# Kernel tuning notes

Hardware: AMD Instinct MI355X
Metric: run time of the kernel (lower is better)

Reference implementation:

```python
import jax, jax.numpy as jnp
import numpy as np

L = 2        # gnn_layers
D = 256      # hidden_dim
E = 1024     # emb_dim
NCLS = 7
NEG = 1e30


def lstm_cell(x, h, c, Wih, Whh, bih, bhh):
    # torch.nn.LSTMCell math; gate order i, f, g, o
    g = x @ Wih.T + bih + h @ Whh.T + bhh
    i, f, gg, o = jnp.split(g, 4, axis=-1)
    c2 = jax.nn.sigmoid(f) * c + jax.nn.sigmoid(i) * jnp.tanh(gg)
    return jax.nn.sigmoid(o) * jnp.tanh(c2), c2


def dag_layer(Hl, adj_f, W1, W2, Wr, Wc_ih, Wc_hh, bc_ih, bc_hh, Wp_ih, Wp_hh, bp_ih, bp_hh):
    # Hl: (B,N,D). Sequential DAG recurrence with dot-product attention over growing prefix.
    B, N, Dh = Hl.shape
    zeros = jnp.zeros((B, Dh), Hl.dtype)
    h0 = Hl[:, 0]
    C0, _ = lstm_cell(h0, zeros, zeros, Wc_ih, Wc_hh, bc_ih, bc_hh)
    P0, _ = lstm_cell(zeros, h0, h0, Wp_ih, Wp_hh, bp_ih, bp_hh)
    Ht0 = C0 + P0
    # carry pre-projected keys/values incrementally to avoid O(N^2 D^2) work
    K2 = jnp.zeros((B, N, Dh), Hl.dtype).at[:, 0].set(Ht0 @ W2.T)
    Vr = jnp.zeros((B, N, Dh), Hl.dtype).at[:, 0].set(Ht0 @ Wr.T)
    H1 = jnp.zeros((B, N, Dh), Hl.dtype).at[:, 0].set(Ht0)
    pos = jnp.arange(N)

    def step(carry, i):
        K2, Vr, H1 = carry
        Q = jax.lax.dynamic_index_in_dim(Hl, i, axis=1, keepdims=False)      # (B,D)
        adj_i = jax.lax.dynamic_index_in_dim(adj_f, i, axis=1, keepdims=False)  # (B,N)
        q = Q @ W1.T
        logits = jnp.einsum('bd,bnd->bn', q, K2) - (1.0 - adj_i) * NEG  # mask_logic
        logits = jnp.where(pos[None, :] < i, logits, -NEG)              # only prefix :i
        w = jax.nn.softmax(logits, axis=-1)
        M = jnp.einsum('bn,bnd->bd', w, Vr)
        C, _ = lstm_cell(Q, M, M, Wc_ih, Wc_hh, bc_ih, bc_hh)
        P, _ = lstm_cell(M, Q, Q, Wp_ih, Wp_hh, bp_ih, bp_hh)
        Ht = C + P
        K2 = K2.at[:, i].set(Ht @ W2.T)
        Vr = Vr.at[:, i].set(Ht @ Wr.T)
        H1 = H1.at[:, i].set(Ht)
        return (K2, Vr, H1), None

    (K2, Vr, H1), _ = jax.lax.scan(step, (K2, Vr, H1), jnp.arange(1, N))
    return H1


def setup_inputs() -> dict:
    key = jax.random.key(0)
    ks = iter(jax.random.split(key, 40))
    B, N = 16, 128
    s = lambda *sh: jax.random.normal(next(ks), sh, jnp.float32) * 0.02
    in_dim = D * (L + 1) + E
    return dict(
        features=jax.random.normal(next(ks), (B, N, E), jnp.float32),
        adj=jnp.ones((B, N, N), jnp.int32),
        s_mask=jnp.zeros((B, N, N), jnp.int32),
        s_mask_onehot=jnp.zeros((B, N, N, 2), jnp.int32),
        lengths=jnp.ones((B,), jnp.int32) * N,
        fc1_W=s(D, E), fc1_b=jnp.zeros((D,), jnp.float32),
        W1=s(L, D, D), W2=s(L, D, D), Wr=s(L, D, D),
        Wc_ih=s(L, 4 * D, D), Wc_hh=s(L, 4 * D, D),
        bc_ih=jnp.zeros((L, 4 * D), jnp.float32), bc_hh=jnp.zeros((L, 4 * D), jnp.float32),
        Wp_ih=s(L, 4 * D, D), Wp_hh=s(L, 4 * D, D),
        bp_ih=jnp.zeros((L, 4 * D), jnp.float32), bp_hh=jnp.zeros((L, 4 * D), jnp.float32),
        m0_W=s(D, in_dim), m0_b=jnp.zeros((D,), jnp.float32),
        m1_W=s(D, D), m1_b=jnp.zeros((D,), jnp.float32),
        m2_W=s(NCLS, D), m2_b=jnp.zeros((NCLS,), jnp.float32),
    )


def reference(features, adj, s_mask, s_mask_onehot, lengths,
              fc1_W, fc1_b, W1, W2, Wr,
              Wc_ih, Wc_hh, bc_ih, bc_hh,
              Wp_ih, Wp_hh, bp_ih, bp_hh,
              m0_W, m0_b, m1_W, m1_b, m2_W, m2_b):
    # s_mask / s_mask_onehot unused for attn_type='dotprod', no_rel_attn=True
    # lengths unused for nodal_att_type=None (attentive_node_features is identity)
    adj_f = adj.astype(features.dtype)
    H0 = jax.nn.relu(features @ fc1_W.T + fc1_b)
    Hs = [H0]
    for l in range(L):
        Hs.append(dag_layer(Hs[l], adj_f,
                            W1[l], W2[l], Wr[l],
                            Wc_ih[l], Wc_hh[l], bc_ih[l], bc_hh[l],
                            Wp_ih[l], Wp_hh[l], bp_ih[l], bp_hh[l]))
    Hcat = jnp.concatenate(Hs + [features], axis=2)  # (B,N,D*(L+1)+E)
    h = jax.nn.relu(Hcat @ m0_W.T + m0_b)
    h = jax.nn.relu(h @ m1_W.T + m1_b)  # mlp_layers-1 extra layer; dropout p=0 -> identity
    return h @ m2_W.T + m2_b            # (B,N,num_class)
```

## Files before the change

kernel.cpp:

```cpp
#include <hip/hip_runtime.h>
#include <hip/hip_fp16.h>
#include <math.h>

#define B_ 16
#define N_ 128
#define D_ 256
#define E_ 1024
#define GD4 1024
#define SENT 0xFFC0DEADu

typedef _Float16 h2 __attribute__((ext_vector_type(2)));

__device__ __forceinline__ float dot2w(unsigned w, h2 hv, float acc) {
#if __has_builtin(__builtin_amdgcn_fdot2)
  return __builtin_amdgcn_fdot2(__builtin_bit_cast(h2, w), hv, acc, false);
#else
  union { unsigned u; _Float16 e[2]; } c; c.u = w;
  return acc + (float)c.e[0]*(float)hv.x + (float)c.e[1]*(float)hv.y;
#endif
}
__device__ __forceinline__ float dot2h(h2 a, h2 b, float acc) {
#if __has_builtin(__builtin_amdgcn_fdot2)
  return __builtin_amdgcn_fdot2(a, b, acc, false);
#else
  return acc + (float)a.x*(float)b.x + (float)a.y*(float)b.y;
#endif
}

template<bool BIAS, bool RELU>
__global__ __launch_bounds__(256) void gemm_k(const float* __restrict__ X,
    const float* __restrict__ W, const float* __restrict__ bias,
    float* __restrict__ C, int M, int N, int K)
{
  __shared__ float Xs[32][68];
  __shared__ float Ws[32][68];
  const int tid = threadIdx.x;
  const int m0 = blockIdx.x * 64, n0 = blockIdx.y * 64;
  const int tm = tid >> 4, tn = tid & 15;
  float acc[4][4] = {};
  for (int k0 = 0; k0 < K; k0 += 32) {
    for (int e = tid; e < 2048; e += 256) {
      int mm = e >> 5, kk = e & 31;
      Xs[kk][mm] = X[(m0+mm)*K + k0+kk];
    }
    for (int e = tid; e < 2048; e += 256) {
      int nn = e >> 5, kk = e & 31;
      Ws[kk][nn] = (n0+nn < N) ? W[(n0+nn)*K + k0+kk] : 0.f;
    }
    __syncthreads();
    for (int kk = 0; kk < 32; kk++) {
      float4 a = *(const float4*)&Xs[kk][tm*4];
      float4 b = *(const float4*)&Ws[kk][tn*4];
      acc[0][0] += a.x*b.x; acc[0][1] += a.x*b.y; acc[0][2] += a.x*b.z; acc[0][3] += a.x*b.w;
      acc[1][0] += a.y*b.x; acc[1][1] += a.y*b.y; acc[1][2] += a.y*b.z; acc[1][3] += a.y*b.w;
      acc[2][0] += a.z*b.x; acc[2][1] += a.z*b.y; acc[2][2] += a.z*b.z; acc[2][3] += a.z*b.w;
      acc[3][0] += a.w*b.x; acc[3][1] += a.w*b.y; acc[3][2] += a.w*b.z; acc[3][3] += a.w*b.w;
    }
    __syncthreads();
  }
  for (int i2 = 0; i2 < 4; i2++) {
    int row = m0 + tm*4 + i2;
    for (int j2 = 0; j2 < 4; j2++) {
      int col = n0 + tn*4 + j2;
      if (col < N) {
        float v = acc[i2][j2];
        if (BIAS) v += bias[col];
        if (RELU) v = fmaxf(v, 0.f);
        C[row*N + col] = v;
      }
    }
  }
}

template<bool BIAS, bool RELU>
__global__ __launch_bounds__(256) void gemm16_k(const float* __restrict__ X,
    const float* __restrict__ W, const float* __restrict__ bias,
    float* __restrict__ C, int M, int N, int K)
{
  __shared__ h2 Xs2[16][68];
  __shared__ h2 Ws2[16][68];
  const int tid = threadIdx.x;
  const int m0 = blockIdx.x * 64, n0 = blockIdx.y * 64;
  const int tm = tid >> 4, tn = tid & 15;
  float acc[4][4] = {};
  for (int k0 = 0; k0 < K; k0 += 32) {
    for (int e = tid; e < 1024; e += 256) {
      int mm = e >> 4, p = e & 15;
      const float* xp = &X[(m0+mm)*K + k0 + 2*p];
      h2 t; t.x = (_Float16)xp[0]; t.y = (_Float16)xp[1];
      Xs2[p][mm] = t;
    }
    for (int e = tid; e < 1024; e += 256) {
      int nn = e >> 4, p = e & 15;
      const float* wp = &W[(n0+nn)*K + k0 + 2*p];
      h2 t; t.x = (_Float16)wp[0]; t.y = (_Float16)wp[1];
      Ws2[p][nn] = t;
    }
    __syncthreads();
    #pragma unroll 4
    for (int p = 0; p < 16; ++p) {
      h2 a[4], bb[4];
      *(float4*)a  = *(const float4*)&Xs2[p][tm*4];
      *(float4*)bb = *(const float4*)&Ws2[p][tn*4];
      #pragma unroll
      for (int i2 = 0; i2 < 4; i2++)
        #pragma unroll
        for (int j2 = 0; j2 < 4; j2++)
          acc[i2][j2] = dot2h(a[i2], bb[j2], acc[i2][j2]);
    }
    __syncthreads();
  }
  for (int i2 = 0; i2 < 4; i2++) {
    int row = m0 + tm*4 + i2;
    for (int j2 = 0; j2 < 4; j2++) {
      int col = n0 + tn*4 + j2;
      float v = acc[i2][j2];
      if (BIAS) v += bias[col];
      if (RELU) v = fmaxf(v, 0.f);
      C[row*N + col] = v;
    }
  }
}

__global__ __launch_bounds__(256) void prepamat_k(const float* __restrict__ W2,
    const float* __restrict__ W1, float* __restrict__ AM)
{
  __shared__ float Xs[32][68];
  __shared__ float Ws[32][68];
  const int tid = threadIdx.x;
  const int m0 = blockIdx.x * 64, n0 = blockIdx.y * 64;
  const float* X = W2 + blockIdx.z * 65536;
  const float* W = W1 + blockIdx.z * 65536;
  float* C = AM + blockIdx.z * 65536;
  const int tm = tid >> 4, tn = tid & 15;
  float acc[4][4] = {};
  for (int k0 = 0; k0 < 256; k0 += 32) {
    for (int e = tid; e < 2048; e += 256) {
      int kk = e >> 6, mm = e & 63;
      Xs[kk][mm] = X[(k0+kk)*256 + m0+mm];
    }
    for (int e = tid; e < 2048; e += 256) {
      int kk = e >> 6, nn = e & 63;
      Ws[kk][nn] = W[(k0+kk)*256 + n0+nn];
    }
    __syncthreads();
    for (int kk = 0; kk < 32; kk++) {
      float4 a = *(const float4*)&Xs[kk][tm*4];
      float4 b = *(const float4*)&Ws[kk][tn*4];
      acc[0][0] += a.x*b.x; acc[0][1] += a.x*b.y; acc[0][2] += a.x*b.z; acc[0][3] += a.x*b.w;
      acc[1][0] += a.y*b.x; acc[1][1] += a.y*b.y; acc[1][2] += a.y*b.z; acc[1][3] += a.y*b.w;
      acc[2][0] += a.z*b.x; acc[2][1] += a.z*b.y; acc[2][2] += a.z*b.z; acc[2][3] += a.z*b.w;
      acc[3][0] += a.w*b.x; acc[3][1] += a.w*b.y; acc[3][2] += a.w*b.z; acc[3][3] += a.w*b.w;
    }
    __syncthreads();
  }
  for (int i2 = 0; i2 < 4; i2++)
    for (int j2 = 0; j2 < 4; j2++)
      C[(m0 + tm*4 + i2)*256 + n0 + tn*4 + j2] = acc[i2][j2];
}

__global__ __launch_bounds__(256) void prepnn_k(const float* __restrict__ Wch,
    const float* __restrict__ Wpi, const float* __restrict__ Wr,
    float* __restrict__ OUT)
{
  __shared__ float Xs[32][68];
  __shared__ float Ws[32][68];
  const int tid = threadIdx.x;
  const int m0 = blockIdx.x * 64, n0 = blockIdx.y * 64;
  const int l = blockIdx.z;
  const float* X = (m0 < 1024) ? (Wch + l*262144 + m0*256)
                               : (Wpi + l*262144 + (m0-1024)*256);
  const float* W = Wr + l*65536;
  float* C = OUT + l*524288;
  const int tm = tid >> 4, tn = tid & 15;
  float acc[4][4] = {};
  for (int k0 = 0; k0 < 256; k0 += 32) {
    for (int e = tid; e < 2048; e += 256) {
      int mm = e >> 5, kk = e & 31;
      Xs[kk][mm] = X[mm*256 + k0+kk];
    }
    for (int e = tid; e < 2048; e += 256) {
      int kk = e >> 6, nn = e & 63;
      Ws[kk][nn] = W[(k0+kk)*256 + n0+nn];
    }
    __syncthreads();
    for (int kk = 0; kk < 32; kk++) {
      float4 a = *(const float4*)&Xs[kk][tm*4];
      float4 b = *(const float4*)&Ws[kk][tn*4];
      acc[0][0] += a.x*b.x; acc[0][1] += a.x*b.y; acc[0][2] += a.x*b.z; acc[0][3] += a.x*b.w;
      acc[1][0] += a.y*b.x; acc[1][1] += a.y*b.y; acc[1][2] += a.y*b.z; acc[1][3] += a.y*b.w;
      acc[2][0] += a.z*b.x; acc[2][1] += a.z*b.y; acc[2][2] += a.z*b.z; acc[2][3] += a.z*b.w;
      acc[3][0] += a.w*b.x; acc[3][1] += a.w*b.y; acc[3][2] += a.w*b.z; acc[3][3] += a.w*b.w;
    }
    __syncthreads();
  }
  for (int i2 = 0; i2 < 4; i2++)
    for (int j2 = 0; j2 < 4; j2++)
      C[(m0 + tm*4 + i2)*256 + n0 + tn*4 + j2] = acc[i2][j2];
}

__global__ void bias_sum_k(const float* __restrict__ bci, const float* __restrict__ bch,
                           const float* __restrict__ bpi, const float* __restrict__ bph,
                           float* __restrict__ bcC, float* __restrict__ bpC)
{
  int i = blockIdx.x*256 + threadIdx.x;
  if (i < 2048) { bcC[i] = bci[i] + bch[i]; bpC[i] = bpi[i] + bph[i]; }
}

__global__ void pack_k(const float* __restrict__ wchpi, const float* __restrict__ wr,
                       _Float16* __restrict__ out)
{
  int idx = blockIdx.x*256 + threadIdx.x;
  int l  = idx / 589824; int rem = idx % 589824;
  int sl = rem / 36864;  int rem2 = rem % 36864;
  int cq = rem2 / 1152;  int rem3 = rem2 % 1152;
  int r  = rem3 >> 3;    int e = rem3 & 7;
  int c  = cq*8 + e;
  int g  = r >> 4, dl = r & 15;
  int d  = sl*16 + dl;
  float v;
  if (g < 8) v = wchpi[l*524288 + (g*256 + d)*256 + c];
  else       v = wr[l*65536 + d*256 + c];
  out[idx] = (_Float16)v;
}

__global__ void fill_k(unsigned* __restrict__ a, unsigned* __restrict__ b)
{
  int i = blockIdx.x*256 + threadIdx.x;
  if (i < 524288) {
    __hip_atomic_store(a + i, SENT, __ATOMIC_RELAXED, __HIP_MEMORY_SCOPE_AGENT);
    __hip_atomic_store(b + i, SENT, __ATOMIC_RELAXED, __HIP_MEMORY_SCOPE_AGENT);
  }
}

__global__ __launch_bounds__(256) void prologue16_k(const float* __restrict__ X,
    const float* __restrict__ Wc, const float* __restrict__ Wp,
    const float* __restrict__ Am, const float* __restrict__ bcc,
    const float* __restrict__ bpc, float* __restrict__ GQC,
    float* __restrict__ GQP, float* __restrict__ VM)
{
  __shared__ h2 Xs2[16][68];
  __shared__ h2 Ws2[16][68];
  const int tid = threadIdx.x;
  const int m0 = blockIdx.x * 64;
  const int nt = blockIdx.y;
  const float* W; const float* bias; float* C; int n0; int NC;
  if (nt < 16)      { W = Wc; bias = bcc;     C = GQC; n0 = nt*64;      NC = 1024; }
  else if (nt < 32) { W = Wp; bias = bpc;     C = GQP; n0 = (nt-16)*64; NC = 1024; }
  else              { W = Am; bias = nullptr; C = VM;  n0 = (nt-32)*64; NC = 256;  }
  const int tm = tid >> 4, tn = tid & 15;
  float acc[4][4] = {};
  for (int k0 = 0; k0 < 256; k0 += 32) {
    for (int e = tid; e < 1024; e += 256) {
      int mm = e >> 4, p = e & 15;
      const float* xp = &X[(m0+mm)*256 + k0 + 2*p];
      h2 t; t.x = (_Float16)xp[0]; t.y = (_Float16)xp[1];
      Xs2[p][mm] = t;
    }
    for (int e = tid; e < 1024; e += 256) {
      int nn = e >> 4, p = e & 15;
      const float* wp = &W[(n0+nn)*256 + k0 + 2*p];
      h2 t; t.x = (_Float16)wp[0]; t.y = (_Float16)wp[1];
      Ws2[p][nn] = t;
    }
    __syncthreads();
    #pragma unroll 4
    for (int p = 0; p < 16; ++p) {
      h2 a[4], bb[4];
      *(float4*)a  = *(const float4*)&Xs2[p][tm*4];
      *(float4*)bb = *(const float4*)&Ws2[p][tn*4];
      #pragma unroll
      for (int i2 = 0; i2 < 4; i2++)
        #pragma unroll
        for (int j2 = 0; j2 < 4; j2++)
          acc[i2][j2] = dot2h(a[i2], bb[j2], acc[i2][j2]);
    }
    __syncthreads();
  }
  for (int i2 = 0; i2 < 4; i2++) {
    int row = m0 + tm*4 + i2;
    for (int j2 = 0; j2 < 4; j2++) {
      int col = n0 + tn*4 + j2;
      float v = acc[i2][j2];
      if (bias) v += bias[col];
      C[row*NC + col] = v;
    }
  }
}

__global__ __launch_bounds__(256) void m0fused16_k(const float* __restrict__ H0,
    const float* __restrict__ H1, const float* __restrict__ H2,
    const float* __restrict__ feat, const float* __restrict__ W,
    const float* __restrict__ bias, float* __restrict__ C)
{
  __shared__ h2 Xs2[16][68];
  __shared__ h2 Ws2[16][68];
  const int tid = threadIdx.x;
  const int m0 = blockIdx.x * 64, n0 = blockIdx.y * 64;
  const int tm = tid >> 4, tn = tid & 15;
  float acc[4][4] = {};
  for (int k0 = 0; k0 < 1792; k0 += 32) {
    for (int e = tid; e < 1024; e += 256) {
      int mm = e >> 4, p = e & 15;
      int k = k0 + 2*p, row = m0 + mm;
      float x0, x1;
      if (k < 768) {
        const float* src = (k < 256) ? H0 : ((k < 512) ? H1 : H2);
        x0 = src[row*256 + (k & 255)];
        x1 = src[row*256 + (k & 255) + 1];
      } else {
        x0 = feat[row*1024 + (k - 768)];
        x1 = feat[row*1024 + (k - 767)];
      }
      h2 t; t.x = (_Float16)x0; t.y = (_Float16)x1;
      Xs2[p][mm] = t;
    }
    for (int e = tid; e < 1024; e += 256) {
      int nn = e >> 4, p = e & 15;
      const float* wp = &W[(n0+nn)*1792 + k0 + 2*p];
      h2 t; t.x = (_Float16)wp[0]; t.y = (_Float16)wp[1];
      Ws2[p][nn] = t;
    }
    __syncthreads();
    #pragma unroll 4
    for (int p = 0; p < 16; ++p) {
      h2 a[4], bb[4];
      *(float4*)a  = *(const float4*)&Xs2[p][tm*4];
      *(float4*)bb = *(const float4*)&Ws2[p][tn*4];
      #pragma unroll
      for (int i2 = 0; i2 < 4; i2++)
        #pragma unroll
        for (int j2 = 0; j2 < 4; j2++)
          acc[i2][j2] = dot2h(a[i2], bb[j2], acc[i2][j2]);
    }
    __syncthreads();
  }
  for (int i2 = 0; i2 < 4; i2++) {
    int row = m0 + tm*4 + i2;
    for (int j2 = 0; j2 < 4; j2++) {
      int col = n0 + tn*4 + j2;
      C[row*256 + col] = fmaxf(acc[i2][j2] + bias[col], 0.f);
    }
  }
}

__device__ __forceinline__ float sigf(float x) { return 1.f / (1.f + __expf(-x)); }
__device__ __forceinline__ float tanhfast(float x) {
  float xc = fminf(fmaxf(x, -15.f), 15.f);
  float e = __expf(-2.f * xc);
  return (1.f - e) / (1.f + e);
}

__global__ __launch_bounds__(512, 2) void scan_k(
    const float* __restrict__ Hl,
    const float* __restrict__ Vm,
    const float* __restrict__ gqC,
    const float* __restrict__ gqP,
    const _Float16* __restrict__ WTp,
    const int*   __restrict__ adj,
    float* __restrict__ Hout)
{
  __shared__ uint4 wl4[4608];
  __shared__ float G[128*144];
  __shared__ __align__(16) _Float16 h2s[256];
  __shared__ float v_s[256];
  __shared__ __align__(16) _Float16 v2s[256];
  __shared__ float psum[128];
  __shared__ float aw[128];
  __shared__ int   adj_s[2][128];
  __shared__ float gqc_l[2][64], gqp_l[2][64];
  __shared__ float ql[2][16];
  __shared__ float Gg[144];
  __shared__ float red[2];
  __shared__ float sinv;

  const int tid = threadIdx.x;
  const int b   = blockIdx.x >> 4;
  const int sl  = blockIdx.x & 15;

  { const uint4* src = (const uint4*)WTp + (size_t)sl*4608;
    for (int e = tid; e < 4608; e += 512) wl4[e] = src[e]; }

  const int rr_ = tid >> 2;
  const int rj  = tid & 3;

#define PREF(ip_, bf_) do {                                                    \
    int ip = (ip_); int bf = (bf_);                                            \
    for (int u = tid - 288; u < 528; u += 224) {                               \
      if (u < 256) { float v = Vm[(b*N_ + ip)*D_ + u]; v_s[u] = v;             \
                     v2s[u] = (_Float16)v; }                                   \
      else if (u < 384) adj_s[bf][u-256] = adj[(b*N_ + ip)*N_ + (u-256)];      \
      else if (u < 448) gqc_l[bf][u-384] = gqC[(b*N_+ip)*GD4 + ((u-384)>>4)*D_ + sl*16 + ((u-384)&15)]; \
      else if (u < 512) gqp_l[bf][u-448] = gqP[(b*N_+ip)*GD4 + ((u-448)>>4)*D_ + sl*16 + ((u-448)&15)]; \
      else ql[bf][u-512] = Hl[(b*N_+ip)*D_ + sl*16 + (u-512)];                 \
    }                                                                          \
  } while (0)

  if (tid >= 288) PREF(0, 0);
  __syncthreads();

  for (int i = 0; i < N_; ++i) {
    const int cur = i & 1;
    if (i > 0) {
      if (rr_ + 1 < i) {
        const float4* hp = (const float4*)(Hout + ((size_t)(b*N_ + rr_))*D_) + rj;
        const float4* vv = (const float4*)v_s + rj;
        float4 areg[16];
        #pragma unroll
        for (int c4 = 0; c4 < 16; ++c4) areg[c4] = hp[c4*4];
        float acc = 0.f;
        #pragma unroll
        for (int c4 = 0; c4 < 16; ++c4) {
          float4 a = areg[c4], w = vv[c4*4];
          acc += a.x*w.x + a.y*w.y + a.z*w.z + a.w*w.w;
        }
        acc += __shfl_xor(acc, 1, 64);
        acc += __shfl_xor(acc, 2, 64);
        if (rj == 0) psum[rr_] = acc;
      }
      if (tid >= 448) {
        const unsigned* wp = (const unsigned*)Hout
                           + ((size_t)(b*N_ + (i-1)))*D_ + ((tid-448)&15)*16 + 15;
        while (__hip_atomic_load(wp, __ATOMIC_RELAXED, __HIP_MEMORY_SCOPE_AGENT) == SENT)
          __builtin_amdgcn_s_sleep(1);
        int lane = tid - 448;
        float4 hv = *((const float4*)(Hout + ((size_t)(b*N_ + (i-1)))*D_) + lane);
        h2* hd = (h2*)h2s + lane*2;
        h2 t0; t0.x = (_Float16)hv.x; t0.y = (_Float16)hv.y;
        h2 t1; t1.x = (_Float16)hv.z; t1.y = (_Float16)hv.w;
        hd[0] = t0; hd[1] = t1;
      }
      __syncthreads();
      asm volatile("" ::: "memory");

      if (tid < 288) {
        int r = tid >> 1, hf = tid & 1;
        float acc2 = 0.f;
        #pragma unroll 4
        for (int it = 0; it < 16; ++it) {
          int cq = hf*16 + it;
          uint4 w4 = wl4[cq*144 + r];
          const h2* hh = (const h2*)h2s + cq*4;
          acc2 = dot2w(w4.x, hh[0], acc2);
          acc2 = dot2w(w4.y, hh[1], acc2);
          acc2 = dot2w(w4.z, hh[2], acc2);
          acc2 = dot2w(w4.w, hh[3], acc2);
        }
        acc2 += __shfl_xor(acc2, 1, 64);
        if (!hf) G[(i-1)*144 + r] = acc2;
      }
      if (rr_ == i-1) {
        const h2* hh = (const h2*)h2s + rj*32;
        const h2* vv = (const h2*)v2s + rj*32;
        float acc = 0.f;
        #pragma unroll 8
        for (int q = 0; q < 32; ++q) acc = dot2h(hh[q], vv[q], acc);
        acc += __shfl_xor(acc, 1, 64);
        acc += __shfl_xor(acc, 2, 64);
        if (rj == 0) psum[i-1] = acc;
      }
      if (tid >= 320 && tid < 448) {
        int k = tid - 320;
        float e = (k + 1 < i && adj_s[cur][k] != 0) ? __expf(psum[k]) : 0.f;
        aw[k] = e;
        float sv = e;
        #pragma unroll
        for (int off = 32; off >= 1; off >>= 1) sv += __shfl_xor(sv, off, 64);
        if ((k & 63) == 0) red[k >> 6] = sv;
      }
      __syncthreads();

      if (tid < 288) {
        int r = tid >> 1, kh = tid & 1;
        float e1 = (adj_s[cur][i-1] != 0) ? __expf(psum[i-1]) : 0.f;
        float g = kh ? e1 * G[(i-1)*144 + r] : 0.f;
        int m = i - 1;
        int k0 = kh ? (m >> 1) : 0, k1 = kh ? m : (m >> 1);
        for (int k = k0; k < k1; ++k) g += aw[k] * G[k*144 + r];
        g += __shfl_xor(g, 1, 64);
        if (!kh) Gg[r] = g;
        if (tid == 0) sinv = 1.f / (red[0] + red[1] + e1);
      } else {
        PREF((i < 127) ? i+1 : 127, (i+1) & 1);
      }
      __syncthreads();
    } else {
      if (tid >= 288) PREF(1, 1);
      __syncthreads();
    }

    if (tid < 32) {
      int dl = tid >> 1, cell = tid & 1;
      float inv = (i > 0) ? sinv : 0.f;
      float r0 = 0.f, r1 = 0.f, r2 = 0.f, r3 = 0.f, Mv = 0.f;
      if (i > 0) {
        r0 = Gg[(cell*4+0)*16 + dl] * inv;
        r1 = Gg[(cell*4+1)*16 + dl] * inv;
        r2 = Gg[(cell*4+2)*16 + dl] * inv;
        r3 = Gg[(cell*4+3)*16 + dl] * inv;
        Mv = Gg[128 + dl] * inv;
      }
      float Qv = ql[cur][dl];
      const float* gq = cell ? &gqp_l[cur][0] : &gqc_l[cur][0];
      float xi = cell ? Qv : Mv;
      float gi_ = r0 + gq[ 0 + dl];
      float gf_ = r1 + gq[16 + dl];
      float gg_ = r2 + gq[32 + dl];
      float go_ = r3 + gq[48 + dl];
      float c2  = sigf(gf_)*xi + sigf(gi_)*tanhfast(gg_);
      float ov  = sigf(go_)*tanhfast(c2);
      float htv = ov + __shfl_xor(ov, 1, 64);
      if (!cell) {
        __hip_atomic_store(&Hout[((size_t)(b*N_ + i))*D_ + sl*16 + dl], htv,
                           __ATOMIC_RELAXED, __HIP_MEMORY_SCOPE_AGENT);
      }
    }
  }
#undef PREF
}

extern "C" void kernel_launch(void* const* d_in, const int* in_sizes, int n_in,
                              void* d_out, int out_size, void* d_ws, size_t ws_size,
                              hipStream_t stream)
{
  const float* features = (const float*)d_in[0];
  const int*   adj      = (const int*)  d_in[1];
  const float* fc1_W    = (const float*)d_in[5];
  const float* fc1_b    = (const float*)d_in[6];
  const float* W1       = (const float*)d_in[7];
  const float* W2       = (const float*)d_in[8];
  const float* Wr       = (const float*)d_in[9];
  const float* Wc_ih    = (const float*)d_in[10];
  const float* Wc_hh    = (const float*)d_in[11];
  const float* bc_ih    = (const float*)d_in[12];
  const float* bc_hh    = (const float*)d_in[13];
  const float* Wp_ih    = (const float*)d_in[14];
  const float* Wp_hh    = (const float*)d_in[15];
  const float* bp_ih    = (const float*)d_in[16];
  const float* bp_hh    = (const float*)d_in[17];
  const float* m0_W     = (const float*)d_in[18];
  const float* m0_b     = (const float*)d_in[19];
  const float* m1_W     = (const float*)d_in[20];
  const float* m1_b     = (const float*)d_in[21];
  const float* m2_W     = (const float*)d_in[22];
  const float* m2_b     = (const float*)d_in[23];

  float* ws = (float*)d_ws;
  _Float16* WTP = (_Float16*)ws;
  float* AMAT   = ws + 589824;
  float* BCC    = ws + 720896;
  float* BPC    = ws + 722944;
  float* WCHPI  = ws + 724992;
  float* H0     = ws + 1773568;
  float* H1     = ws + 2297856;
  float* H2     = ws + 2822144;
  float* VMAT   = ws + 3346432;
  float* GQC    = ws + 3870720;
  float* GQP    = ws + 5967872;
  float* HB1    = ws + 8065024;
  float* HB2    = ws + 8589312;

  fill_k<<<2048, 256, 0, stream>>>((unsigned*)H1, (unsigned*)H2);
  bias_sum_k<<<8, 256, 0, stream>>>(bc_ih, bc_hh, bp_ih, bp_hh, BCC, BPC);
  prepamat_k<<<dim3(4,4,2), 256, 0, stream>>>(W2, W1, AMAT);
  prepnn_k<<<dim3(32,4,2), 256, 0, stream>>>(Wc_hh, Wp_ih, Wr, WCHPI);
  pack_k<<<4608, 256, 0, stream>>>(WCHPI, Wr, WTP);

  gemm16_k<true,true><<<dim3(32,4), 256, 0, stream>>>(features, fc1_W, fc1_b, H0, 2048, 256, 1024);

  prologue16_k<<<dim3(32,36), 256, 0, stream>>>(H0, Wc_ih, Wp_hh, AMAT,
                                                BCC, BPC, GQC, GQP, VMAT);
  scan_k<<<256, 512, 0, stream>>>(H0, VMAT, GQC, GQP, WTP, adj, H1);

  prologue16_k<<<dim3(32,36), 256, 0, stream>>>(H1, Wc_ih + 262144, Wp_hh + 262144,
                                                AMAT + 65536, BCC + 1024, BPC + 1024,
                                                GQC, GQP, VMAT);
  scan_k<<<256, 512, 0, stream>>>(H1, VMAT, GQC, GQP, WTP + 589824, adj, H2);

  m0fused16_k<<<dim3(32,4), 256, 0, stream>>>(H0, H1, H2, features, m0_W, m0_b, HB1);
  gemm_k<true,true ><<<dim3(32,4), 256, 0, stream>>>(HB1, m1_W, m1_b, HB2, 2048, 256, 256);
  gemm_k<true,false><<<dim3(32,1), 256, 0, stream>>>(HB2, m2_W, m2_b, (float*)d_out, 2048, 7, 256);
}
```

Baseline: 1.819 ms.

## Exchange scan hidden states across blocks via packed fp16 mailbox

Scan blocks now publish each new hidden-state slice twice: fp32 for downstream consumers and a packed fp16 copy in a separate buffer that peers poll. Polling covers every word with a wave-wide ballot instead of waiting on one sentinel per 16-element slice, then reads half the bytes. The same wave computes the newest prefix attention logit during the fetch, which drops a separate dot-product phase and the special-case term for the last row. The risks are fp16 values colliding with the half-precision sentinel and extra store and shuffle work on the critical path.

```diff
diff --git a/kernel.cpp b/kernel.cpp
--- a/kernel.cpp
+++ b/kernel.cpp
@@ -7,7 +7,7 @@
 #define D_ 256
 #define E_ 1024
 #define GD4 1024
-#define SENT 0xFFC0DEADu
+#define SENTH 0xDEADu
 
 typedef _Float16 h2 __attribute__((ext_vector_type(2)));
 
@@ -227,9 +227,10 @@
 __global__ void fill_k(unsigned* __restrict__ a, unsigned* __restrict__ b)
 {
   int i = blockIdx.x*256 + threadIdx.x;
-  if (i < 524288) {
-    __hip_atomic_store(a + i, SENT, __ATOMIC_RELAXED, __HIP_MEMORY_SCOPE_AGENT);
-    __hip_atomic_store(b + i, SENT, __ATOMIC_RELAXED, __HIP_MEMORY_SCOPE_AGENT);
+  if (i < 262144) {
+    unsigned s = (SENTH << 16) | SENTH;
+    __hip_atomic_store(a + i, s, __ATOMIC_RELAXED, __HIP_MEMORY_SCOPE_AGENT);
+    __hip_atomic_store(b + i, s, __ATOMIC_RELAXED, __HIP_MEMORY_SCOPE_AGENT);
   }
 }
 
@@ -358,13 +359,14 @@
     const float* __restrict__ gqP,
     const _Float16* __restrict__ WTp,
     const int*   __restrict__ adj,
-    float* __restrict__ Hout)
+    float* __restrict__ Hout,
+    unsigned* __restrict__ HoutH)
 {
   __shared__ uint4 wl4[4608];
   __shared__ float G[128*144];
-  __shared__ __align__(16) _Float16 h2s[256];
+  __shared__ __align__(8) _Float16 h2s[256];
   __shared__ float v_s[256];
-  __shared__ __align__(16) _Float16 v2s[256];
+  __shared__ __align__(8) _Float16 v2s[256];
   __shared__ float psum[128];
   __shared__ float aw[128];
   __shared__ int   adj_s[2][128];
@@ -372,7 +374,7 @@
   __shared__ float ql[2][16];
   __shared__ float Gg[144];
   __shared__ float red[2];
-  __shared__ float sinv;
+  __shared__ float sinv_s;
 
   const int tid = threadIdx.x;
   const int b   = blockIdx.x >> 4;
@@ -419,16 +421,23 @@
         if (rj == 0) psum[rr_] = acc;
       }
       if (tid >= 448) {
-        const unsigned* wp = (const unsigned*)Hout
-                           + ((size_t)(b*N_ + (i-1)))*D_ + ((tid-448)&15)*16 + 15;
-        while (__hip_atomic_load(wp, __ATOMIC_RELAXED, __HIP_MEMORY_SCOPE_AGENT) == SENT)
-          __builtin_amdgcn_s_sleep(1);
-        int lane = tid - 448;
-        float4 hv = *((const float4*)(Hout + ((size_t)(b*N_ + (i-1)))*D_) + lane);
-        h2* hd = (h2*)h2s + lane*2;
-        h2 t0; t0.x = (_Float16)hv.x; t0.y = (_Float16)hv.y;
-        h2 t1; t1.x = (_Float16)hv.z; t1.y = (_Float16)hv.w;
-        hd[0] = t0; hd[1] = t1;
+        int L = tid - 448;
+        const unsigned* hp = HoutH + ((size_t)(b*N_ + (i-1)))*128 + 2*L;
+        unsigned u0, u1;
+        do {
+          u0 = __hip_atomic_load(hp + 0, __ATOMIC_RELAXED, __HIP_MEMORY_SCOPE_AGENT);
+          u1 = __hip_atomic_load(hp + 1, __ATOMIC_RELAXED, __HIP_MEMORY_SCOPE_AGENT);
+        } while (__ballot(((u0 >> 16) == SENTH) || ((u1 >> 16) == SENTH)));
+        ((unsigned*)h2s)[2*L + 0] = u0;
+        ((unsigned*)h2s)[2*L + 1] = u1;
+        h2 hv0 = __builtin_bit_cast(h2, u0);
+        h2 hv1 = __builtin_bit_cast(h2, u1);
+        h2 vv0 = ((const h2*)v2s)[2*L + 0];
+        h2 vv1 = ((const h2*)v2s)[2*L + 1];
+        float p = dot2h(hv1, vv1, dot2h(hv0, vv0, 0.f));
+        #pragma unroll
+        for (int off = 32; off >= 1; off >>= 1) p += __shfl_xor(p, off, 64);
+        if (L == 0) psum[i-1] = p;
       }
       __syncthreads();
       asm volatile("" ::: "memory");
@@ -449,19 +458,9 @@
         acc2 += __shfl_xor(acc2, 1, 64);
         if (!hf) G[(i-1)*144 + r] = acc2;
       }
-      if (rr_ == i-1) {
-        const h2* hh = (const h2*)h2s + rj*32;
-        const h2* vv = (const h2*)v2s + rj*32;
-        float acc = 0.f;
-        #pragma unroll 8
-        for (int q = 0; q < 32; ++q) acc = dot2h(hh[q], vv[q], acc);
-        acc += __shfl_xor(acc, 1, 64);
-        acc += __shfl_xor(acc, 2, 64);
-        if (rj == 0) psum[i-1] = acc;
-      }
       if (tid >= 320 && tid < 448) {
         int k = tid - 320;
-        float e = (k + 1 < i && adj_s[cur][k] != 0) ? __expf(psum[k]) : 0.f;
+        float e = (k < i && adj_s[cur][k] != 0) ? __expf(psum[k]) : 0.f;
         aw[k] = e;
         float sv = e;
         #pragma unroll
@@ -472,14 +471,12 @@
 
       if (tid < 288) {
         int r = tid >> 1, kh = tid & 1;
-        float e1 = (adj_s[cur][i-1] != 0) ? __expf(psum[i-1]) : 0.f;
-        float g = kh ? e1 * G[(i-1)*144 + r] : 0.f;
-        int m = i - 1;
-        int k0 = kh ? (m >> 1) : 0, k1 = kh ? m : (m >> 1);
+        int k0 = kh ? (i >> 1) : 0, k1 = kh ? i : (i >> 1);
+        float g = 0.f;
         for (int k = k0; k < k1; ++k) g += aw[k] * G[k*144 + r];
         g += __shfl_xor(g, 1, 64);
         if (!kh) Gg[r] = g;
-        if (tid == 0) sinv = 1.f / (red[0] + red[1] + e1);
+        if (tid == 0) sinv_s = 1.f / (red[0] + red[1]);
       } else {
         PREF((i < 127) ? i+1 : 127, (i+1) & 1);
       }
@@ -491,7 +488,7 @@
 
     if (tid < 32) {
       int dl = tid >> 1, cell = tid & 1;
-      float inv = (i > 0) ? sinv : 0.f;
+      float inv = (i > 0) ? sinv_s : 0.f;
       float r0 = 0.f, r1 = 0.f, r2 = 0.f, r3 = 0.f, Mv = 0.f;
       if (i > 0) {
         r0 = Gg[(cell*4+0)*16 + dl] * inv;
@@ -513,6 +510,14 @@
       if (!cell) {
         __hip_atomic_store(&Hout[((size_t)(b*N_ + i))*D_ + sl*16 + dl], htv,
                            __ATOMIC_RELAXED, __HIP_MEMORY_SCOPE_AGENT);
+      }
+      float hnx = __shfl(htv, tid + 2, 64);
+      if ((tid & 3) == 0) {
+        union { _Float16 h[2]; unsigned u; } pk;
+        pk.h[0] = (_Float16)htv;
+        pk.h[1] = (_Float16)hnx;
+        __hip_atomic_store(HoutH + ((size_t)(b*N_ + i))*128 + sl*8 + (tid >> 2),
+                           pk.u, __ATOMIC_RELAXED, __HIP_MEMORY_SCOPE_AGENT);
       }
     }
   }
@@ -559,8 +564,10 @@
   float* GQP    = ws + 5967872;
   float* HB1    = ws + 8065024;
   float* HB2    = ws + 8589312;
-
-  fill_k<<<2048, 256, 0, stream>>>((unsigned*)H1, (unsigned*)H2);
+  unsigned* H1H = (unsigned*)(ws + 9113600);
+  unsigned* H2H = (unsigned*)(ws + 9375744);
+
+  fill_k<<<1024, 256, 0, stream>>>(H1H, H2H);
   bias_sum_k<<<8, 256, 0, stream>>>(bc_ih, bc_hh, bp_ih, bp_hh, BCC, BPC);
   prepamat_k<<<dim3(4,4,2), 256, 0, stream>>>(W2, W1, AMAT);
   prepnn_k<<<dim3(32,4,2), 256, 0, stream>>>(Wc_hh, Wp_ih, Wr, WCHPI);
@@ -570,12 +577,12 @@
 
   prologue16_k<<<dim3(32,36), 256, 0, stream>>>(H0, Wc_ih, Wp_hh, AMAT,
                                                 BCC, BPC, GQC, GQP, VMAT);
-  scan_k<<<256, 512, 0, stream>>>(H0, VMAT, GQC, GQP, WTP, adj, H1);
+  scan_k<<<256, 512, 0, stream>>>(H0, VMAT, GQC, GQP, WTP, adj, H1, H1H);
 
   prologue16_k<<<dim3(32,36), 256, 0, stream>>>(H1, Wc_ih + 262144, Wp_hh + 262144,
                                                 AMAT + 65536, BCC + 1024, BPC + 1024,
                                                 GQC, GQP, VMAT);
-  scan_k<<<256, 512, 0, stream>>>(H1, VMAT, GQC, GQP, WTP + 589824, adj, H2);
+  scan_k<<<256, 512, 0, stream>>>(H1, VMAT, GQC, GQP, WTP + 589824, adj, H2, H2H);
 
   m0fused16_k<<<dim3(32,4), 256, 0, stream>>>(H0, H1, H2, features, m0_W, m0_b, HB1);
   gemm_k<true,true ><<<dim3(32,4), 256, 0, stream>>>(HB1, m1_W, m1_b, HB2, 2048, 256, 256);
```

New measurement: 1.873 ms. +3.0%, slower.

## Replace dot2-based fp16 GEMMs with MFMA 16x16x32 matrix-core kernels

Applied to the files above, without the earlier changes.

Rewrites the fc1, prologue, m0 and m1 GEMMs to stage 64x256 fp16 tiles in LDS and compute with MFMA 16x16x32 f16 instructions, four waves each owning a 32x32 output block. The goal is to remove the VALU-bound fdot2 inner loops and the small-K staging loop overhead. It uses much more LDS per block, which can lower occupancy. It also lowers the alignment of two scan shared buffers.

```diff
diff --git a/kernel.cpp b/kernel.cpp
--- a/kernel.cpp
+++ b/kernel.cpp
@@ -10,6 +10,8 @@
 #define SENT 0xFFC0DEADu
 
 typedef _Float16 h2 __attribute__((ext_vector_type(2)));
+typedef _Float16 f16x8 __attribute__((ext_vector_type(8)));
+typedef float f32x4 __attribute__((ext_vector_type(4)));
 
 __device__ __forceinline__ float dot2w(unsigned w, h2 hv, float acc) {
 #if __has_builtin(__builtin_amdgcn_fdot2)
@@ -72,54 +74,150 @@
   }
 }
 
+__device__ __forceinline__ void mf_stage(const float* __restrict__ src,
+    int ldsrc, _Float16 (*dst)[264], int tid)
+{
+  for (int e = tid; e < 8192; e += 256) {
+    int row = e >> 7, cp = e & 127;
+    float2 v = *(const float2*)&src[(size_t)row*ldsrc + 2*cp];
+    h2 t; t.x = (_Float16)v.x; t.y = (_Float16)v.y;
+    *(h2*)&dst[row][2*cp] = t;
+  }
+}
+
+__device__ __forceinline__ void mf_compute(_Float16 (*Xh)[264],
+    _Float16 (*Wh)[264], f32x4 acc[2][2], int l, int wr, int wc)
+{
+  #pragma unroll
+  for (int kc = 0; kc < 256; kc += 32) {
+    f16x8 a0 = *(const f16x8*)&Xh[wr*32 +      (l & 15)][kc + (l >> 4)*8];
+    f16x8 a1 = *(const f16x8*)&Xh[wr*32 + 16 + (l & 15)][kc + (l >> 4)*8];
+    f16x8 b0 = *(const f16x8*)&Wh[wc*32 +      (l & 15)][kc + (l >> 4)*8];
+    f16x8 b1 = *(const f16x8*)&Wh[wc*32 + 16 + (l & 15)][kc + (l >> 4)*8];
+    acc[0][0] = __builtin_amdgcn_mfma_f32_16x16x32_f16(a0, b0, acc[0][0], 0, 0, 0);
+    acc[0][1] = __builtin_amdgcn_mfma_f32_16x16x32_f16(a0, b1, acc[0][1], 0, 0, 0);
+    acc[1][0] = __builtin_amdgcn_mfma_f32_16x16x32_f16(a1, b0, acc[1][0], 0, 0, 0);
+    acc[1][1] = __builtin_amdgcn_mfma_f32_16x16x32_f16(a1, b1, acc[1][1], 0, 0, 0);
+  }
+}
+
 template<bool BIAS, bool RELU>
-__global__ __launch_bounds__(256) void gemm16_k(const float* __restrict__ X,
+__global__ __launch_bounds__(256) void mfgemm_k(const float* __restrict__ X,
     const float* __restrict__ W, const float* __restrict__ bias,
     float* __restrict__ C, int M, int N, int K)
 {
-  __shared__ h2 Xs2[16][68];
-  __shared__ h2 Ws2[16][68];
+  __shared__ _Float16 Xh[64][264];
+  __shared__ _Float16 Wh[64][264];
   const int tid = threadIdx.x;
   const int m0 = blockIdx.x * 64, n0 = blockIdx.y * 64;
-  const int tm = tid >> 4, tn = tid & 15;
-  float acc[4][4] = {};
-  for (int k0 = 0; k0 < K; k0 += 32) {
-    for (int e = tid; e < 1024; e += 256) {
-      int mm = e >> 4, p = e & 15;
-      const float* xp = &X[(m0+mm)*K + k0 + 2*p];
-      h2 t; t.x = (_Float16)xp[0]; t.y = (_Float16)xp[1];
-      Xs2[p][mm] = t;
-    }
-    for (int e = tid; e < 1024; e += 256) {
-      int nn = e >> 4, p = e & 15;
-      const float* wp = &W[(n0+nn)*K + k0 + 2*p];
-      h2 t; t.x = (_Float16)wp[0]; t.y = (_Float16)wp[1];
-      Ws2[p][nn] = t;
-    }
-    __syncthreads();
-    #pragma unroll 4
-    for (int p = 0; p < 16; ++p) {
-      h2 a[4], bb[4];
-      *(float4*)a  = *(const float4*)&Xs2[p][tm*4];
-      *(float4*)bb = *(const float4*)&Ws2[p][tn*4];
+  const int l = tid & 63, w = tid >> 6;
+  const int wr = w >> 1, wc = w & 1;
+  f32x4 acc[2][2];
+  #pragma unroll
+  for (int rt = 0; rt < 2; ++rt)
+    #pragma unroll
+    for (int ct = 0; ct < 2; ++ct) acc[rt][ct] = 0.f;
+  for (int k0 = 0; k0 < K; k0 += 256) {
+    mf_stage(X + (size_t)m0*K + k0, K, Xh, tid);
+    mf_stage(W + (size_t)n0*K + k0, K, Wh, tid);
+    __syncthreads();
+    mf_compute(Xh, Wh, acc, l, wr, wc);
+    __syncthreads();
+  }
+  #pragma unroll
+  for (int rt = 0; rt < 2; ++rt)
+    #pragma unroll
+    for (int ct = 0; ct < 2; ++ct)
       #pragma unroll
-      for (int i2 = 0; i2 < 4; i2++)
-        #pragma unroll
-        for (int j2 = 0; j2 < 4; j2++)
-          acc[i2][j2] = dot2h(a[i2], bb[j2], acc[i2][j2]);
-    }
-    __syncthreads();
-  }
-  for (int i2 = 0; i2 < 4; i2++) {
-    int row = m0 + tm*4 + i2;
-    for (int j2 = 0; j2 < 4; j2++) {
-      int col = n0 + tn*4 + j2;
-      float v = acc[i2][j2];
-      if (BIAS) v += bias[col];
-      if (RELU) v = fmaxf(v, 0.f);
-      C[row*N + col] = v;
-    }
-  }
+      for (int j = 0; j < 4; ++j) {
+        int row = m0 + wr*32 + rt*16 + (l >> 4)*4 + j;
+        int col = n0 + wc*32 + ct*16 + (l & 15);
+        float v = acc[rt][ct][j];
+        if (BIAS) v += bias[col];
+        if (RELU) v = fmaxf(v, 0.f);
+        C[(size_t)row*N + col] = v;
+      }
+}
+
+__global__ __launch_bounds__(256) void prologue_mf_k(const float* __restrict__ X,
+    const float* __restrict__ Wc, const float* __restrict__ Wp,
+    const float* __restrict__ Am, const float* __restrict__ bcc,
+    const float* __restrict__ bpc, float* __restrict__ GQC,
+    float* __restrict__ GQP, float* __restrict__ VM)
+{
+  __shared__ _Float16 Xh[64][264];
+  __shared__ _Float16 Wh[64][264];
+  const int tid = threadIdx.x;
+  const int m0 = blockIdx.x * 64;
+  const int nt = blockIdx.y;
+  const float* W; const float* bias; float* C; int n0; int NC;
+  if (nt < 16)      { W = Wc; bias = bcc;     C = GQC; n0 = nt*64;      NC = 1024; }
+  else if (nt < 32) { W = Wp; bias = bpc;     C = GQP; n0 = (nt-16)*64; NC = 1024; }
+  else              { W = Am; bias = nullptr; C = VM;  n0 = (nt-32)*64; NC = 256;  }
+  const int l = tid & 63, w = tid >> 6;
+  const int wr = w >> 1, wc = w & 1;
+  f32x4 acc[2][2];
+  #pragma unroll
+  for (int rt = 0; rt < 2; ++rt)
+    #pragma unroll
+    for (int ct = 0; ct < 2; ++ct) acc[rt][ct] = 0.f;
+  mf_stage(X + (size_t)m0*256, 256, Xh, tid);
+  mf_stage(W + (size_t)n0*256, 256, Wh, tid);
+  __syncthreads();
+  mf_compute(Xh, Wh, acc, l, wr, wc);
+  __syncthreads();
+  #pragma unroll
+  for (int rt = 0; rt < 2; ++rt)
+    #pragma unroll
+    for (int ct = 0; ct < 2; ++ct)
+      #pragma unroll
+      for (int j = 0; j < 4; ++j) {
+        int row = m0 + wr*32 + rt*16 + (l >> 4)*4 + j;
+        int col = n0 + wc*32 + ct*16 + (l & 15);
+        float v = acc[rt][ct][j];
+        if (bias) v += bias[col];
+        C[(size_t)row*NC + col] = v;
+      }
+}
+
+__global__ __launch_bounds__(256) void m0fused_mf_k(const float* __restrict__ H0,
+    const float* __restrict__ H1, const float* __restrict__ H2,
+    const float* __restrict__ feat, const float* __restrict__ W,
+    const float* __restrict__ bias, float* __restrict__ C)
+{
+  __shared__ _Float16 Xh[64][264];
+  __shared__ _Float16 Wh[64][264];
+  const int tid = threadIdx.x;
+  const int m0 = blockIdx.x * 64, n0 = blockIdx.y * 64;
+  const int l = tid & 63, w = tid >> 6;
+  const int wr = w >> 1, wc = w & 1;
+  f32x4 acc[2][2];
+  #pragma unroll
+  for (int rt = 0; rt < 2; ++rt)
+    #pragma unroll
+    for (int ct = 0; ct < 2; ++ct) acc[rt][ct] = 0.f;
+  for (int k0 = 0; k0 < 1792; k0 += 256) {
+    const float* src; int lds_; int coff;
+    if (k0 == 0)        { src = H0;   lds_ = 256;  coff = 0; }
+    else if (k0 == 256) { src = H1;   lds_ = 256;  coff = 0; }
+    else if (k0 == 512) { src = H2;   lds_ = 256;  coff = 0; }
+    else                { src = feat; lds_ = 1024; coff = k0 - 768; }
+    mf_stage(src + (size_t)m0*lds_ + coff, lds_, Xh, tid);
+    mf_stage(W + (size_t)n0*1792 + k0, 1792, Wh, tid);
+    __syncthreads();
+    mf_compute(Xh, Wh, acc, l, wr, wc);
+    __syncthreads();
+  }
+  #pragma unroll
+  for (int rt = 0; rt < 2; ++rt)
+    #pragma unroll
+    for (int ct = 0; ct < 2; ++ct)
+      #pragma unroll
+      for (int j = 0; j < 4; ++j) {
+        int row = m0 + wr*32 + rt*16 + (l >> 4)*4 + j;
+        int col = n0 + wc*32 + ct*16 + (l & 15);
+        C[(size_t)row*256 + col] = fmaxf(acc[rt][ct][j] + bias[col], 0.f);
+      }
 }
 
 __global__ __launch_bounds__(256) void prepamat_k(const float* __restrict__ W2,
@@ -233,117 +331,6 @@
   }
 }
 
-__global__ __launch_bounds__(256) void prologue16_k(const float* __restrict__ X,
-    const float* __restrict__ Wc, const float* __restrict__ Wp,
-    const float* __restrict__ Am, const float* __restrict__ bcc,
-    const float* __restrict__ bpc, float* __restrict__ GQC,
-    float* __restrict__ GQP, float* __restrict__ VM)
-{
-  __shared__ h2 Xs2[16][68];
-  __shared__ h2 Ws2[16][68];
-  const int tid = threadIdx.x;
-  const int m0 = blockIdx.x * 64;
-  const int nt = blockIdx.y;
-  const float* W; const float* bias; float* C; int n0; int NC;
-  if (nt < 16)      { W = Wc; bias = bcc;     C = GQC; n0 = nt*64;      NC = 1024; }
-  else if (nt < 32) { W = Wp; bias = bpc;     C = GQP; n0 = (nt-16)*64; NC = 1024; }
-  else              { W = Am; bias = nullptr; C = VM;  n0 = (nt-32)*64; NC = 256;  }
-  const int tm = tid >> 4, tn = tid & 15;
-  float acc[4][4] = {};
-  for (int k0 = 0; k0 < 256; k0 += 32) {
-    for (int e = tid; e < 1024; e += 256) {
-      int mm = e >> 4, p = e & 15;
-      const float* xp = &X[(m0+mm)*256 + k0 + 2*p];
-      h2 t; t.x = (_Float16)xp[0]; t.y = (_Float16)xp[1];
-      Xs2[p][mm] = t;
-    }
-    for (int e = tid; e < 1024; e += 256) {
-      int nn = e >> 4, p = e & 15;
-      const float* wp = &W[(n0+nn)*256 + k0 + 2*p];
-      h2 t; t.x = (_Float16)wp[0]; t.y = (_Float16)wp[1];
-      Ws2[p][nn] = t;
-    }
-    __syncthreads();
-    #pragma unroll 4
-    for (int p = 0; p < 16; ++p) {
-      h2 a[4], bb[4];
-      *(float4*)a  = *(const float4*)&Xs2[p][tm*4];
-      *(float4*)bb = *(const float4*)&Ws2[p][tn*4];
-      #pragma unroll
-      for (int i2 = 0; i2 < 4; i2++)
-        #pragma unroll
-        for (int j2 = 0; j2 < 4; j2++)
-          acc[i2][j2] = dot2h(a[i2], bb[j2], acc[i2][j2]);
-    }
-    __syncthreads();
-  }
-  for (int i2 = 0; i2 < 4; i2++) {
-    int row = m0 + tm*4 + i2;
-    for (int j2 = 0; j2 < 4; j2++) {
-      int col = n0 + tn*4 + j2;
-      float v = acc[i2][j2];
-      if (bias) v += bias[col];
-      C[row*NC + col] = v;
-    }
-  }
-}
-
-__global__ __launch_bounds__(256) void m0fused16_k(const float* __restrict__ H0,
-    const float* __restrict__ H1, const float* __restrict__ H2,
-    const float* __restrict__ feat, const float* __restrict__ W,
-    const float* __restrict__ bias, float* __restrict__ C)
-{
-  __shared__ h2 Xs2[16][68];
-  __shared__ h2 Ws2[16][68];
-  const int tid = threadIdx.x;
-  const int m0 = blockIdx.x * 64, n0 = blockIdx.y * 64;
-  const int tm = tid >> 4, tn = tid & 15;
-  float acc[4][4] = {};
-  for (int k0 = 0; k0 < 1792; k0 += 32) {
-    for (int e = tid; e < 1024; e += 256) {
-      int mm = e >> 4, p = e & 15;
-      int k = k0 + 2*p, row = m0 + mm;
-      float x0, x1;
-      if (k < 768) {
-        const float* src = (k < 256) ? H0 : ((k < 512) ? H1 : H2);
-        x0 = src[row*256 + (k & 255)];
-        x1 = src[row*256 + (k & 255) + 1];
-      } else {
-        x0 = feat[row*1024 + (k - 768)];
-        x1 = feat[row*1024 + (k - 767)];
-      }
-      h2 t; t.x = (_Float16)x0; t.y = (_Float16)x1;
-      Xs2[p][mm] = t;
-    }
-    for (int e = tid; e < 1024; e += 256) {
-      int nn = e >> 4, p = e & 15;
-      const float* wp = &W[(n0+nn)*1792 + k0 + 2*p];
-      h2 t; t.x = (_Float16)wp[0]; t.y = (_Float16)wp[1];
-      Ws2[p][nn] = t;
-    }
-    __syncthreads();
-    #pragma unroll 4
-    for (int p = 0; p < 16; ++p) {
-      h2 a[4], bb[4];
-      *(float4*)a  = *(const float4*)&Xs2[p][tm*4];
-      *(float4*)bb = *(const float4*)&Ws2[p][tn*4];
-      #pragma unroll
-      for (int i2 = 0; i2 < 4; i2++)
-        #pragma unroll
-        for (int j2 = 0; j2 < 4; j2++)
-          acc[i2][j2] = dot2h(a[i2], bb[j2], acc[i2][j2]);
-    }
-    __syncthreads();
-  }
-  for (int i2 = 0; i2 < 4; i2++) {
-    int row = m0 + tm*4 + i2;
-    for (int j2 = 0; j2 < 4; j2++) {
-      int col = n0 + tn*4 + j2;
-      C[row*256 + col] = fmaxf(acc[i2][j2] + bias[col], 0.f);
-    }
-  }
-}
-
 __device__ __forceinline__ float sigf(float x) { return 1.f / (1.f + __expf(-x)); }
 __device__ __forceinline__ float tanhfast(float x) {
   float xc = fminf(fmaxf(x, -15.f), 15.f);
@@ -362,9 +349,9 @@
 {
   __shared__ uint4 wl4[4608];
   __shared__ float G[128*144];
-  __shared__ __align__(16) _Float16 h2s[256];
+  __shared__ __align__(8) _Float16 h2s[256];
   __shared__ float v_s[256];
-  __shared__ __align__(16) _Float16 v2s[256];
+  __shared__ __align__(8) _Float16 v2s[256];
   __shared__ float psum[128];
   __shared__ float aw[128];
   __shared__ int   adj_s[2][128];
@@ -566,18 +553,18 @@
   prepnn_k<<<dim3(32,4,2), 256, 0, stream>>>(Wc_hh, Wp_ih, Wr, WCHPI);
   pack_k<<<4608, 256, 0, stream>>>(WCHPI, Wr, WTP);
 
-  gemm16_k<true,true><<<dim3(32,4), 256, 0, stream>>>(features, fc1_W, fc1_b, H0, 2048, 256, 1024);
-
-  prologue16_k<<<dim3(32,36), 256, 0, stream>>>(H0, Wc_ih, Wp_hh, AMAT,
-                                                BCC, BPC, GQC, GQP, VMAT);
+  mfgemm_k<true,true><<<dim3(32,4), 256, 0, stream>>>(features, fc1_W, fc1_b, H0, 2048, 256, 1024);
+
+  prologue_mf_k<<<dim3(32,36), 256, 0, stream>>>(H0, Wc_ih, Wp_hh, AMAT,
+                                                 BCC, BPC, GQC, GQP, VMAT);
   scan_k<<<256, 512, 0, stream>>>(H0, VMAT, GQC, GQP, WTP, adj, H1);
 
-  prologue16_k<<<dim3(32,36), 256, 0, stream>>>(H1, Wc_ih + 262144, Wp_hh + 262144,
-                                                AMAT + 65536, BCC + 1024, BPC + 1024,
-                                                GQC, GQP, VMAT);
+  prologue_mf_k<<<dim3(32,36), 256, 0, stream>>>(H1, Wc_ih + 262144, Wp_hh + 262144,
+                                                 AMAT + 65536, BCC + 1024, BPC + 1024,
+                                                 GQC, GQP, VMAT);
   scan_k<<<256, 512, 0, stream>>>(H1, VMAT, GQC, GQP, WTP + 589824, adj, H2);
 
-  m0fused16_k<<<dim3(32,4), 256, 0, stream>>>(H0, H1, H2, features, m0_W, m0_b, HB1);
-  gemm_k<true,true ><<<dim3(32,4), 256, 0, stream>>>(HB1, m1_W, m1_b, HB2, 2048, 256, 256);
+  m0fused_mf_k<<<dim3(32,4), 256, 0, stream>>>(H0, H1, H2, features, m0_W, m0_b, HB1);
+  mfgemm_k<true,true><<<dim3(32,4), 256, 0, stream>>>(HB1, m1_W, m1_b, HB2, 2048, 256, 256);
   gemm_k<true,false><<<dim3(32,1), 256, 0, stream>>>(HB2, m2_W, m2_b, (float*)d_out, 2048, 7, 256);
 }
```

New measurement: 1.785 ms. No clear change (-1.9%).
